# Kernel optimization log

Hardware: AMD Instinct MI355X
Metric: run time of the kernel (lower is better)

The kernel has to match this reference:

```python
import jax, jax.numpy as jnp
import numpy as np


def setup_inputs() -> dict:
    key = jax.random.key(0)
    k1, k2, k3 = jax.random.split(key, 3)
    B, D, H, W, K = 16, 512, 60, 60, 32
    std = 1.0 / np.sqrt(K * D)
    X = jax.random.normal(k1, (B, D, H, W), dtype=jnp.float32)
    codewords = jax.random.uniform(k2, (K, D), dtype=jnp.float32, minval=-std, maxval=std)
    # scale is drawn uniform(-1, 0) in the torch module (shake in train mode)
    scale = -jax.random.uniform(k3, (K,), dtype=jnp.float32)
    return {"X": X, "codewords": codewords, "scale": scale}


def reference(X, codewords, scale):
    # X: (B, D, H, W) -> flatten spatial to (B, N, D)
    B, D = X.shape[0], X.shape[1]
    Xf = X.reshape(B, D, -1).transpose(0, 2, 1)          # (B, N, D)
    # scaledL2: SL[b,n,k] = scale[k] * ||X[b,n] - C[k]||^2, expanded via GEMM
    # to avoid the (B, N, K, D) residual tensor.
    x2 = jnp.sum(Xf * Xf, axis=-1)                       # (B, N)
    c2 = jnp.sum(codewords * codewords, axis=-1)         # (K,)
    xc = jnp.einsum('bnd,kd->bnk', Xf, codewords)        # (B, N, K)
    sl = scale * (x2[..., None] - 2.0 * xc + c2)         # (B, N, K)
    A = jax.nn.softmax(sl, axis=2)                       # (B, N, K)
    # aggregate: E[b,k,d] = sum_n A[b,n,k] * (X[b,n,d] - C[k,d])
    E = jnp.einsum('bnk,bnd->bkd', A, Xf) - jnp.sum(A, axis=1)[..., None] * codewords
    return E                                             # (B, K, D)
```

## Files before the change

### kernel.cpp

```cpp
#include <hip/hip_runtime.h>
#include <hip/hip_bf16.h>

constexpr int BB = 16;
constexpr int DD = 512;
constexpr int NN = 3600;
constexpr int KK = 32;
constexpr int SB = 29;
constexpr int WIN = 128;

typedef __attribute__((ext_vector_type(8))) short short8;
typedef __attribute__((ext_vector_type(4))) float f32x4;

__device__ inline unsigned bf16pack(float a, float b) {
    unsigned ia = __float_as_uint(a), ib = __float_as_uint(b);
    ia = (ia + 0x7fffu + ((ia >> 16) & 1u)) >> 16;
    ib = (ib + 0x7fffu + ((ib >> 16) & 1u)) & 0xffff0000u;
    return ia | ib;
}

__global__ __launch_bounds__(256) void k0_prep(const float* __restrict__ Cw,
                                               const float* __restrict__ scale,
                                               ushort* __restrict__ Cbf,
                                               float* __restrict__ sc2) {
    __shared__ float buf[8][32];
    const int t = threadIdx.x;
    const int k = t & 31;
    const int h = t >> 5;
    const float4* row = reinterpret_cast<const float4*>(Cw + k * DD + h * 64);
    uint2* crow = reinterpret_cast<uint2*>(Cbf + k * DD + h * 64);
    float s = 0.f;
#pragma unroll
    for (int j = 0; j < 16; ++j) {
        float4 v = row[j];
        crow[j] = make_uint2(bf16pack(v.x, v.y), bf16pack(v.z, v.w));
        s += v.x * v.x + v.y * v.y + v.z * v.z + v.w * v.w;
    }
    buf[h][k] = s;
    __syncthreads();
    if (t < 32) {
        float tot = 0.f;
#pragma unroll
        for (int j = 0; j < 8; ++j) tot += buf[j][t];
        sc2[t] = scale[t] * tot;
    }
}

__global__ __launch_bounds__(512) void kf_fused(const float* __restrict__ X,
                                                const ushort* __restrict__ Cbf,
                                                const float* __restrict__ scale,
                                                const float* __restrict__ sc2,
                                                float* __restrict__ Ep,
                                                float* __restrict__ asum_part) {
    __shared__ ushort tile[DD * WIN];
    __shared__ ushort As2[KK * WIN];
    __shared__ float x2part[16][WIN];
    __shared__ float x2s[WIN];
    __shared__ float asw[8][KK];

    const int t = threadIdx.x;
    const int w = t >> 6;
    const int l = t & 63;
    const int q = l >> 4;
    const int r = l & 15;
    const int b = blockIdx.x / SB;
    const int sb = blockIdx.x % SB;
    const int n0 = sb * WIN;

    const int ng = t & 31;
    const int dgs = t >> 5;
    int nst = n0 + ng * 4;
    if (nst > NN - 4) nst = NN - 4;
    const float* xsrc = X + (size_t)b * DD * NN + nst;

    const ushort* cb0 = Cbf + r * DD + q * 8;
    const ushort* cb1 = cb0 + 16 * DD;
    const int nloc = w * 16 + r;

    float x2loc[4] = {0.f, 0.f, 0.f, 0.f};
    f32x4 a0 = {0.f, 0.f, 0.f, 0.f};
    f32x4 a1 = {0.f, 0.f, 0.f, 0.f};

    float4 cur[4];
#pragma unroll
    for (int i = 0; i < 4; ++i)
        cur[i] = *reinterpret_cast<const float4*>(xsrc + (size_t)(dgs * 4 + i) * NN);

#pragma unroll
    for (int j = 0; j < 8; ++j) {
        float4 nxt[4];
        if (j < 7) {
#pragma unroll
            for (int i = 0; i < 4; ++i)
                nxt[i] = *reinterpret_cast<const float4*>(
                    xsrc + (size_t)((j + 1) * 64 + dgs * 4 + i) * NN);
        }
#pragma unroll
        for (int i = 0; i < 4; ++i) {
            const float4 v = cur[i];
            x2loc[0] = fmaf(v.x, v.x, x2loc[0]);
            x2loc[1] = fmaf(v.y, v.y, x2loc[1]);
            x2loc[2] = fmaf(v.z, v.z, x2loc[2]);
            x2loc[3] = fmaf(v.w, v.w, x2loc[3]);
            const int d = j * 64 + dgs * 4 + i;
            *reinterpret_cast<uint2*>(&tile[d * 128 + ((ng * 4) ^ ((d & 7) << 3))]) =
                make_uint2(bf16pack(v.x, v.y), bf16pack(v.z, v.w));
        }
        __syncthreads();
#pragma unroll
        for (int u = 0; u < 2; ++u) {
            const int s = 2 * j + u;
            union { short8 s8; ushort us[8]; } af;
#pragma unroll
            for (int jj = 0; jj < 8; ++jj) {
                const int d = s * 32 + q * 8 + jj;
                af.us[jj] = tile[d * 128 + (nloc ^ (jj << 3))];
            }
            const short8 c0 = *reinterpret_cast<const short8*>(cb0 + s * 32);
            const short8 c1 = *reinterpret_cast<const short8*>(cb1 + s * 32);
            a0 = __builtin_amdgcn_mfma_f32_16x16x32_bf16(af.s8, c0, a0, 0, 0, 0);
            a1 = __builtin_amdgcn_mfma_f32_16x16x32_bf16(af.s8, c1, a1, 0, 0, 0);
        }
        if (j < 7) {
#pragma unroll
            for (int i = 0; i < 4; ++i) cur[i] = nxt[i];
        }
    }

    *reinterpret_cast<f32x4*>(&x2part[dgs][ng * 4]) =
        (f32x4){x2loc[0], x2loc[1], x2loc[2], x2loc[3]};
    __syncthreads();
    if (t < WIN) {
        float s = 0.f;
#pragma unroll
        for (int dg = 0; dg < 16; ++dg) s += x2part[dg][t];
        x2s[t] = s;
    }
    __syncthreads();

    const float sk0 = scale[r], sk1 = scale[r + 16];
    const float sq0 = sc2[r],  sq1 = sc2[r + 16];
    float e0v[4], e1v[4];
    float as0 = 0.f, as1 = 0.f;
#pragma unroll
    for (int i = 0; i < 4; ++i) {
        const float x2v = x2s[w * 16 + 4 * q + i];
        float sl0 = fmaf(sk0, x2v, sq0) - 2.f * sk0 * a0[i];
        float sl1 = fmaf(sk1, x2v, sq1) - 2.f * sk1 * a1[i];
        float m = fmaxf(sl0, sl1);
        m = fmaxf(m, __shfl_xor(m, 1));
        m = fmaxf(m, __shfl_xor(m, 2));
        m = fmaxf(m, __shfl_xor(m, 4));
        m = fmaxf(m, __shfl_xor(m, 8));
        float e0 = __expf(sl0 - m), e1 = __expf(sl1 - m);
        float ssum = e0 + e1;
        ssum += __shfl_xor(ssum, 1);
        ssum += __shfl_xor(ssum, 2);
        ssum += __shfl_xor(ssum, 4);
        ssum += __shfl_xor(ssum, 8);
        const float inv = 1.f / ssum;
        e0 *= inv; e1 *= inv;
        if (n0 + w * 16 + 4 * q + i >= NN) { e0 = 0.f; e1 = 0.f; }
        e0v[i] = e0; e1v[i] = e1;
        as0 += e0; as1 += e1;
    }
    *reinterpret_cast<uint2*>(&As2[r * 128 + ((w * 16 + 4 * q) ^ ((r & 7) << 3))]) =
        make_uint2(bf16pack(e0v[0], e0v[1]), bf16pack(e0v[2], e0v[3]));
    *reinterpret_cast<uint2*>(&As2[(r + 16) * 128 + ((w * 16 + 4 * q) ^ ((r & 7) << 3))]) =
        make_uint2(bf16pack(e1v[0], e1v[1]), bf16pack(e1v[2], e1v[3]));

    as0 += __shfl_xor(as0, 16); as0 += __shfl_xor(as0, 32);
    as1 += __shfl_xor(as1, 16); as1 += __shfl_xor(as1, 32);
    if (l < 16) { asw[w][r] = as0; asw[w][r + 16] = as1; }
    __syncthreads();
    if (t < KK) {
        float s = 0.f;
#pragma unroll
        for (int jw = 0; jw < 8; ++jw) s += asw[jw][t];
        asum_part[((size_t)b * SB + sb) * KK + t] = s;
    }

    short8 bfr0[4], bfr1[4];
#pragma unroll
    for (int step = 0; step < 4; ++step) {
        bfr0[step] = *reinterpret_cast<const short8*>(
            &As2[r * 128 + ((step * 32 + q * 8) ^ ((r & 7) << 3))]);
        bfr1[step] = *reinterpret_cast<const short8*>(
            &As2[(r + 16) * 128 + ((step * 32 + q * 8) ^ ((r & 7) << 3))]);
    }

    f32x4 acc[4][2];
#pragma unroll
    for (int df = 0; df < 4; ++df) {
        acc[df][0] = (f32x4){0.f, 0.f, 0.f, 0.f};
        acc[df][1] = (f32x4){0.f, 0.f, 0.f, 0.f};
    }

#pragma unroll
    for (int df = 0; df < 4; ++df) {
        const int d = w * 64 + df * 16 + r;
#pragma unroll
        for (int step = 0; step < 4; ++step) {
            const short8 xa = *reinterpret_cast<const short8*>(
                &tile[d * 128 + ((step * 32 + q * 8) ^ ((r & 7) << 3))]);
            acc[df][0] = __builtin_amdgcn_mfma_f32_16x16x32_bf16(
                xa, bfr0[step], acc[df][0], 0, 0, 0);
            acc[df][1] = __builtin_amdgcn_mfma_f32_16x16x32_bf16(
                xa, bfr1[step], acc[df][1], 0, 0, 0);
        }
    }

    float* ep = Ep + (size_t)(b * SB + sb) * KK * DD;
#pragma unroll
    for (int df = 0; df < 4; ++df) {
#pragma unroll
        for (int kf = 0; kf < 2; ++kf) {
            const int k = kf * 16 + r;
            const int d = w * 64 + df * 16 + q * 4;
            *reinterpret_cast<f32x4*>(ep + (size_t)k * DD + d) = acc[df][kf];
        }
    }
}

__global__ __launch_bounds__(256) void k3_final(const float* __restrict__ Ep,
                                                const float* __restrict__ asum_part,
                                                const float* __restrict__ Cw,
                                                float* __restrict__ E) {
    const int t = threadIdx.x;
    const int b = blockIdx.x >> 5, k = blockIdx.x & 31;

    float asum = 0.f;
#pragma unroll
    for (int sb = 0; sb < SB; ++sb)
        asum += asum_part[((size_t)b * SB + sb) * KK + k];

#pragma unroll
    for (int h = 0; h < 2; ++h) {
        const int d = t + h * 256;
        float s2 = 0.f;
#pragma unroll 4
        for (int sb = 0; sb < SB; ++sb)
            s2 += Ep[(((size_t)b * SB + sb) * KK + k) * DD + d];
        E[((size_t)b * KK + k) * DD + d] = s2 - asum * Cw[k * DD + d];
    }
}

extern "C" void kernel_launch(void* const* d_in, const int* in_sizes, int n_in,
                              void* d_out, int out_size, void* d_ws, size_t ws_size,
                              hipStream_t stream) {
    const float* X     = (const float*)d_in[0];
    const float* Cw    = (const float*)d_in[1];
    const float* scale = (const float*)d_in[2];
    float* E = (float*)d_out;

    float* ws = (float*)d_ws;
    float* Ep = ws;
    float* asum_part = Ep + (size_t)BB * SB * KK * DD;
    float* sc2 = asum_part + (size_t)BB * SB * KK;
    ushort* Cbf = (ushort*)(sc2 + KK);

    k0_prep<<<dim3(1), dim3(256), 0, stream>>>(Cw, scale, Cbf, sc2);
    kf_fused<<<dim3(BB * SB), dim3(512), 0, stream>>>(X, Cbf, scale, sc2, Ep, asum_part);
    k3_final<<<dim3(BB * KK), dim3(256), 0, stream>>>(Ep, asum_part, Cw, E);
}
```

Measured before the change: 59.51 us.

## Halve block size and LDS tile, process each 128-point window in two passes

The fused kernel now runs 256 threads per block. Each block handles its 128 spatial positions as two 64-wide passes, keeping the aggregation accumulators in registers across both passes. The LDS tile shrinks from 128 KB to about 68 KB, with padded strides (68/72) replacing the XOR swizzle. The intent is to fit more blocks per CU and raise occupancy. In exchange each wave holds twice the accumulators, so register pressure rises, and each pass adds barriers with less latency hiding per block.

```diff
diff --git a/kernel.cpp b/kernel.cpp
--- a/kernel.cpp
+++ b/kernel.cpp
@@ -6,7 +6,10 @@
 constexpr int NN = 3600;
 constexpr int KK = 32;
 constexpr int SB = 29;
-constexpr int WIN = 128;
+constexpr int WIN = 64;
+constexpr int PASSES = 2;
+constexpr int TS = 68;
+constexpr int AS = 72;
 
 typedef __attribute__((ext_vector_type(8))) short short8;
 typedef __attribute__((ext_vector_type(4))) float f32x4;
@@ -45,177 +48,178 @@
     }
 }
 
-__global__ __launch_bounds__(512) void kf_fused(const float* __restrict__ X,
+__global__ __launch_bounds__(256) void kf_fused(const float* __restrict__ X,
                                                 const ushort* __restrict__ Cbf,
                                                 const float* __restrict__ scale,
                                                 const float* __restrict__ sc2,
                                                 float* __restrict__ Ep,
                                                 float* __restrict__ asum_part) {
-    __shared__ ushort tile[DD * WIN];
-    __shared__ ushort As2[KK * WIN];
+    __shared__ ushort tile[DD * TS];
+    __shared__ ushort As2[KK * AS];
     __shared__ float x2part[16][WIN];
     __shared__ float x2s[WIN];
-    __shared__ float asw[8][KK];
+    __shared__ float asw[4][KK];
 
     const int t = threadIdx.x;
     const int w = t >> 6;
     const int l = t & 63;
     const int q = l >> 4;
     const int r = l & 15;
+    const int ng = t & 15;
+    const int dd = t >> 4;
     const int b = blockIdx.x / SB;
     const int sb = blockIdx.x % SB;
-    const int n0 = sb * WIN;
-
-    const int ng = t & 31;
-    const int dgs = t >> 5;
-    int nst = n0 + ng * 4;
-    if (nst > NN - 4) nst = NN - 4;
-    const float* xsrc = X + (size_t)b * DD * NN + nst;
-
+    const float* Xb = X + (size_t)b * DD * NN;
     const ushort* cb0 = Cbf + r * DD + q * 8;
     const ushort* cb1 = cb0 + 16 * DD;
-    const int nloc = w * 16 + r;
-
-    float x2loc[4] = {0.f, 0.f, 0.f, 0.f};
-    f32x4 a0 = {0.f, 0.f, 0.f, 0.f};
-    f32x4 a1 = {0.f, 0.f, 0.f, 0.f};
-
-    float4 cur[4];
-#pragma unroll
-    for (int i = 0; i < 4; ++i)
-        cur[i] = *reinterpret_cast<const float4*>(xsrc + (size_t)(dgs * 4 + i) * NN);
-
-#pragma unroll
-    for (int j = 0; j < 8; ++j) {
-        float4 nxt[4];
-        if (j < 7) {
-#pragma unroll
-            for (int i = 0; i < 4; ++i)
-                nxt[i] = *reinterpret_cast<const float4*>(
-                    xsrc + (size_t)((j + 1) * 64 + dgs * 4 + i) * NN);
-        }
-#pragma unroll
-        for (int i = 0; i < 4; ++i) {
-            const float4 v = cur[i];
-            x2loc[0] = fmaf(v.x, v.x, x2loc[0]);
-            x2loc[1] = fmaf(v.y, v.y, x2loc[1]);
-            x2loc[2] = fmaf(v.z, v.z, x2loc[2]);
-            x2loc[3] = fmaf(v.w, v.w, x2loc[3]);
-            const int d = j * 64 + dgs * 4 + i;
-            *reinterpret_cast<uint2*>(&tile[d * 128 + ((ng * 4) ^ ((d & 7) << 3))]) =
-                make_uint2(bf16pack(v.x, v.y), bf16pack(v.z, v.w));
-        }
-        __syncthreads();
-#pragma unroll
-        for (int u = 0; u < 2; ++u) {
-            const int s = 2 * j + u;
-            union { short8 s8; ushort us[8]; } af;
-#pragma unroll
-            for (int jj = 0; jj < 8; ++jj) {
-                const int d = s * 32 + q * 8 + jj;
-                af.us[jj] = tile[d * 128 + (nloc ^ (jj << 3))];
-            }
-            const short8 c0 = *reinterpret_cast<const short8*>(cb0 + s * 32);
-            const short8 c1 = *reinterpret_cast<const short8*>(cb1 + s * 32);
-            a0 = __builtin_amdgcn_mfma_f32_16x16x32_bf16(af.s8, c0, a0, 0, 0, 0);
-            a1 = __builtin_amdgcn_mfma_f32_16x16x32_bf16(af.s8, c1, a1, 0, 0, 0);
-        }
-        if (j < 7) {
-#pragma unroll
-            for (int i = 0; i < 4; ++i) cur[i] = nxt[i];
-        }
-    }
-
-    *reinterpret_cast<f32x4*>(&x2part[dgs][ng * 4]) =
-        (f32x4){x2loc[0], x2loc[1], x2loc[2], x2loc[3]};
-    __syncthreads();
-    if (t < WIN) {
-        float s = 0.f;
-#pragma unroll
-        for (int dg = 0; dg < 16; ++dg) s += x2part[dg][t];
-        x2s[t] = s;
-    }
-    __syncthreads();
-
     const float sk0 = scale[r], sk1 = scale[r + 16];
     const float sq0 = sc2[r],  sq1 = sc2[r + 16];
-    float e0v[4], e1v[4];
-    float as0 = 0.f, as1 = 0.f;
-#pragma unroll
-    for (int i = 0; i < 4; ++i) {
-        const float x2v = x2s[w * 16 + 4 * q + i];
-        float sl0 = fmaf(sk0, x2v, sq0) - 2.f * sk0 * a0[i];
-        float sl1 = fmaf(sk1, x2v, sq1) - 2.f * sk1 * a1[i];
-        float m = fmaxf(sl0, sl1);
-        m = fmaxf(m, __shfl_xor(m, 1));
-        m = fmaxf(m, __shfl_xor(m, 2));
-        m = fmaxf(m, __shfl_xor(m, 4));
-        m = fmaxf(m, __shfl_xor(m, 8));
-        float e0 = __expf(sl0 - m), e1 = __expf(sl1 - m);
-        float ssum = e0 + e1;
-        ssum += __shfl_xor(ssum, 1);
-        ssum += __shfl_xor(ssum, 2);
-        ssum += __shfl_xor(ssum, 4);
-        ssum += __shfl_xor(ssum, 8);
-        const float inv = 1.f / ssum;
-        e0 *= inv; e1 *= inv;
-        if (n0 + w * 16 + 4 * q + i >= NN) { e0 = 0.f; e1 = 0.f; }
-        e0v[i] = e0; e1v[i] = e1;
-        as0 += e0; as1 += e1;
-    }
-    *reinterpret_cast<uint2*>(&As2[r * 128 + ((w * 16 + 4 * q) ^ ((r & 7) << 3))]) =
-        make_uint2(bf16pack(e0v[0], e0v[1]), bf16pack(e0v[2], e0v[3]));
-    *reinterpret_cast<uint2*>(&As2[(r + 16) * 128 + ((w * 16 + 4 * q) ^ ((r & 7) << 3))]) =
-        make_uint2(bf16pack(e1v[0], e1v[1]), bf16pack(e1v[2], e1v[3]));
-
-    as0 += __shfl_xor(as0, 16); as0 += __shfl_xor(as0, 32);
-    as1 += __shfl_xor(as1, 16); as1 += __shfl_xor(as1, 32);
-    if (l < 16) { asw[w][r] = as0; asw[w][r + 16] = as1; }
+
+    f32x4 acc[8][2];
+#pragma unroll
+    for (int df = 0; df < 8; ++df) {
+        acc[df][0] = (f32x4){0.f, 0.f, 0.f, 0.f};
+        acc[df][1] = (f32x4){0.f, 0.f, 0.f, 0.f};
+    }
+    float as0t = 0.f, as1t = 0.f;
+
+    for (int p = 0; p < PASSES; ++p) {
+        const int n0p = sb * 128 + p * WIN;
+        int nst = n0p + ng * 4;
+        if (nst > NN - 4) nst = NN - 4;
+        const float* xsrc = Xb + nst;
+
+        f32x4 a0 = {0.f, 0.f, 0.f, 0.f};
+        f32x4 a1 = {0.f, 0.f, 0.f, 0.f};
+        float x2loc[4] = {0.f, 0.f, 0.f, 0.f};
+
+        float4 cur[4];
+#pragma unroll
+        for (int i = 0; i < 4; ++i)
+            cur[i] = *reinterpret_cast<const float4*>(xsrc + (size_t)(dd * 4 + i) * NN);
+
+        for (int c = 0; c < 8; ++c) {
+            float4 nxt[4];
+            if (c < 7) {
+#pragma unroll
+                for (int i = 0; i < 4; ++i)
+                    nxt[i] = *reinterpret_cast<const float4*>(
+                        xsrc + (size_t)((c + 1) * 64 + dd * 4 + i) * NN);
+            }
+#pragma unroll
+            for (int i = 0; i < 4; ++i) {
+                const float4 v = cur[i];
+                x2loc[0] = fmaf(v.x, v.x, x2loc[0]);
+                x2loc[1] = fmaf(v.y, v.y, x2loc[1]);
+                x2loc[2] = fmaf(v.z, v.z, x2loc[2]);
+                x2loc[3] = fmaf(v.w, v.w, x2loc[3]);
+                const int d = c * 64 + dd * 4 + i;
+                *reinterpret_cast<uint2*>(&tile[d * TS + ng * 4]) =
+                    make_uint2(bf16pack(v.x, v.y), bf16pack(v.z, v.w));
+            }
+            __syncthreads();
+#pragma unroll
+            for (int u = 0; u < 2; ++u) {
+                const int s = 2 * c + u;
+                union { short8 s8; ushort us[8]; } af;
+#pragma unroll
+                for (int jj = 0; jj < 8; ++jj)
+                    af.us[jj] = tile[(s * 32 + q * 8 + jj) * TS + w * 16 + r];
+                const short8 c0 = *reinterpret_cast<const short8*>(cb0 + s * 32);
+                const short8 c1 = *reinterpret_cast<const short8*>(cb1 + s * 32);
+                a0 = __builtin_amdgcn_mfma_f32_16x16x32_bf16(af.s8, c0, a0, 0, 0, 0);
+                a1 = __builtin_amdgcn_mfma_f32_16x16x32_bf16(af.s8, c1, a1, 0, 0, 0);
+            }
+            if (c < 7) {
+#pragma unroll
+                for (int i = 0; i < 4; ++i) cur[i] = nxt[i];
+            }
+        }
+
+        *reinterpret_cast<f32x4*>(&x2part[dd][ng * 4]) =
+            (f32x4){x2loc[0], x2loc[1], x2loc[2], x2loc[3]};
+        __syncthreads();
+        if (t < WIN) {
+            float s = 0.f;
+#pragma unroll
+            for (int dg = 0; dg < 16; ++dg) s += x2part[dg][t];
+            x2s[t] = s;
+        }
+        __syncthreads();
+
+        float e0v[4], e1v[4];
+#pragma unroll
+        for (int i = 0; i < 4; ++i) {
+            const float x2v = x2s[w * 16 + 4 * q + i];
+            float sl0 = fmaf(sk0, x2v, sq0) - 2.f * sk0 * a0[i];
+            float sl1 = fmaf(sk1, x2v, sq1) - 2.f * sk1 * a1[i];
+            float m = fmaxf(sl0, sl1);
+            m = fmaxf(m, __shfl_xor(m, 1));
+            m = fmaxf(m, __shfl_xor(m, 2));
+            m = fmaxf(m, __shfl_xor(m, 4));
+            m = fmaxf(m, __shfl_xor(m, 8));
+            float e0 = __expf(sl0 - m), e1 = __expf(sl1 - m);
+            float ssum = e0 + e1;
+            ssum += __shfl_xor(ssum, 1);
+            ssum += __shfl_xor(ssum, 2);
+            ssum += __shfl_xor(ssum, 4);
+            ssum += __shfl_xor(ssum, 8);
+            const float inv = 1.f / ssum;
+            e0 *= inv; e1 *= inv;
+            if (n0p + w * 16 + 4 * q + i >= NN) { e0 = 0.f; e1 = 0.f; }
+            e0v[i] = e0; e1v[i] = e1;
+            as0t += e0; as1t += e1;
+        }
+        *reinterpret_cast<uint2*>(&As2[r * AS + w * 16 + 4 * q]) =
+            make_uint2(bf16pack(e0v[0], e0v[1]), bf16pack(e0v[2], e0v[3]));
+        *reinterpret_cast<uint2*>(&As2[(r + 16) * AS + w * 16 + 4 * q]) =
+            make_uint2(bf16pack(e1v[0], e1v[1]), bf16pack(e1v[2], e1v[3]));
+        __syncthreads();
+
+        short8 bfr0[2], bfr1[2];
+#pragma unroll
+        for (int step = 0; step < 2; ++step) {
+            bfr0[step] = *reinterpret_cast<const short8*>(
+                &As2[r * AS + step * 32 + q * 8]);
+            bfr1[step] = *reinterpret_cast<const short8*>(
+                &As2[(r + 16) * AS + step * 32 + q * 8]);
+        }
+#pragma unroll
+        for (int df = 0; df < 8; ++df) {
+            const int d = w * 128 + df * 16 + r;
+#pragma unroll
+            for (int step = 0; step < 2; ++step) {
+                union { short8 s8; uint2 u2[2]; } xa;
+                const ushort* tp = &tile[d * TS + step * 32 + q * 8];
+                xa.u2[0] = *reinterpret_cast<const uint2*>(tp);
+                xa.u2[1] = *reinterpret_cast<const uint2*>(tp + 4);
+                acc[df][0] = __builtin_amdgcn_mfma_f32_16x16x32_bf16(
+                    xa.s8, bfr0[step], acc[df][0], 0, 0, 0);
+                acc[df][1] = __builtin_amdgcn_mfma_f32_16x16x32_bf16(
+                    xa.s8, bfr1[step], acc[df][1], 0, 0, 0);
+            }
+        }
+        __syncthreads();
+    }
+
+    as0t += __shfl_xor(as0t, 16); as0t += __shfl_xor(as0t, 32);
+    as1t += __shfl_xor(as1t, 16); as1t += __shfl_xor(as1t, 32);
+    if (l < 16) { asw[w][r] = as0t; asw[w][r + 16] = as1t; }
     __syncthreads();
     if (t < KK) {
         float s = 0.f;
 #pragma unroll
-        for (int jw = 0; jw < 8; ++jw) s += asw[jw][t];
+        for (int jw = 0; jw < 4; ++jw) s += asw[jw][t];
         asum_part[((size_t)b * SB + sb) * KK + t] = s;
     }
 
-    short8 bfr0[4], bfr1[4];
-#pragma unroll
-    for (int step = 0; step < 4; ++step) {
-        bfr0[step] = *reinterpret_cast<const short8*>(
-            &As2[r * 128 + ((step * 32 + q * 8) ^ ((r & 7) << 3))]);
-        bfr1[step] = *reinterpret_cast<const short8*>(
-            &As2[(r + 16) * 128 + ((step * 32 + q * 8) ^ ((r & 7) << 3))]);
-    }
-
-    f32x4 acc[4][2];
-#pragma unroll
-    for (int df = 0; df < 4; ++df) {
-        acc[df][0] = (f32x4){0.f, 0.f, 0.f, 0.f};
-        acc[df][1] = (f32x4){0.f, 0.f, 0.f, 0.f};
-    }
-
-#pragma unroll
-    for (int df = 0; df < 4; ++df) {
-        const int d = w * 64 + df * 16 + r;
-#pragma unroll
-        for (int step = 0; step < 4; ++step) {
-            const short8 xa = *reinterpret_cast<const short8*>(
-                &tile[d * 128 + ((step * 32 + q * 8) ^ ((r & 7) << 3))]);
-            acc[df][0] = __builtin_amdgcn_mfma_f32_16x16x32_bf16(
-                xa, bfr0[step], acc[df][0], 0, 0, 0);
-            acc[df][1] = __builtin_amdgcn_mfma_f32_16x16x32_bf16(
-                xa, bfr1[step], acc[df][1], 0, 0, 0);
-        }
-    }
-
     float* ep = Ep + (size_t)(b * SB + sb) * KK * DD;
 #pragma unroll
-    for (int df = 0; df < 4; ++df) {
+    for (int df = 0; df < 8; ++df) {
 #pragma unroll
         for (int kf = 0; kf < 2; ++kf) {
             const int k = kf * 16 + r;
-            const int d = w * 64 + df * 16 + q * 4;
+            const int d = w * 128 + df * 16 + q * 4;
             *reinterpret_cast<f32x4*>(ep + (size_t)k * DD + d) = acc[df][kf];
         }
     }
@@ -259,6 +263,6 @@
     ushort* Cbf = (ushort*)(sc2 + KK);
 
     k0_prep<<<dim3(1), dim3(256), 0, stream>>>(Cw, scale, Cbf, sc2);
-    kf_fused<<<dim3(BB * SB), dim3(512), 0, stream>>>(X, Cbf, scale, sc2, Ep, asum_part);
+    kf_fused<<<dim3(BB * SB), dim3(256), 0, stream>>>(X, Cbf, scale, sc2, Ep, asum_part);
     k3_final<<<dim3(BB * KK), dim3(256), 0, stream>>>(Ep, asum_part, Cw, E);
 }
```

After: 66.76 us. 12.2% more time.

## Load X in four 128-row chunks with double-buffered prefetch and fewer barriers

Applied to the files above, without the earlier changes.

The first phase now loads X in four chunks of 128 D-rows, each thread holding 8 float4 loads in a ping-pong register buffer, instead of eight chunks of 64 rows. This halves the number of block barriers and puts more global loads in flight per chunk. Codeword fragments are loaded at the top of each chunk, and a raw s_barrier plus sched_barrier replace __syncthreads. Launch bounds now ask for 2 blocks per CU, which raises register pressure from the larger buffers. The swizzle index in the second GEMM changes from (r&7) to (d&7), which is equivalent because d ≡ r mod 8.

```diff
diff --git a/kernel.cpp b/kernel.cpp
--- a/kernel.cpp
+++ b/kernel.cpp
@@ -45,12 +45,12 @@
     }
 }
 
-__global__ __launch_bounds__(512) void kf_fused(const float* __restrict__ X,
-                                                const ushort* __restrict__ Cbf,
-                                                const float* __restrict__ scale,
-                                                const float* __restrict__ sc2,
-                                                float* __restrict__ Ep,
-                                                float* __restrict__ asum_part) {
+__global__ __launch_bounds__(512, 2) void kf_fused(const float* __restrict__ X,
+                                                   const ushort* __restrict__ Cbf,
+                                                   const float* __restrict__ scale,
+                                                   const float* __restrict__ sc2,
+                                                   float* __restrict__ Ep,
+                                                   float* __restrict__ asum_part) {
     __shared__ ushort tile[DD * WIN];
     __shared__ ushort As2[KK * WIN];
     __shared__ float x2part[16][WIN];
@@ -62,69 +62,75 @@
     const int l = t & 63;
     const int q = l >> 4;
     const int r = l & 15;
+    const int ng = t & 31;
+    const int dgs = t >> 5;
     const int b = blockIdx.x / SB;
     const int sb = blockIdx.x % SB;
     const int n0 = sb * WIN;
-
-    const int ng = t & 31;
-    const int dgs = t >> 5;
+    const float* Xb = X + (size_t)b * DD * NN;
+    const ushort* cb0 = Cbf + r * DD + q * 8;
+    const ushort* cb1 = cb0 + 16 * DD;
+
     int nst = n0 + ng * 4;
     if (nst > NN - 4) nst = NN - 4;
-    const float* xsrc = X + (size_t)b * DD * NN + nst;
-
-    const ushort* cb0 = Cbf + r * DD + q * 8;
-    const ushort* cb1 = cb0 + 16 * DD;
+    const float* xsrc = Xb + nst;
+
     const int nloc = w * 16 + r;
-
-    float x2loc[4] = {0.f, 0.f, 0.f, 0.f};
     f32x4 a0 = {0.f, 0.f, 0.f, 0.f};
     f32x4 a1 = {0.f, 0.f, 0.f, 0.f};
-
-    float4 cur[4];
-#pragma unroll
-    for (int i = 0; i < 4; ++i)
-        cur[i] = *reinterpret_cast<const float4*>(xsrc + (size_t)(dgs * 4 + i) * NN);
-
-#pragma unroll
-    for (int j = 0; j < 8; ++j) {
-        float4 nxt[4];
-        if (j < 7) {
-#pragma unroll
-            for (int i = 0; i < 4; ++i)
-                nxt[i] = *reinterpret_cast<const float4*>(
-                    xsrc + (size_t)((j + 1) * 64 + dgs * 4 + i) * NN);
-        }
-#pragma unroll
-        for (int i = 0; i < 4; ++i) {
-            const float4 v = cur[i];
-            x2loc[0] = fmaf(v.x, v.x, x2loc[0]);
-            x2loc[1] = fmaf(v.y, v.y, x2loc[1]);
-            x2loc[2] = fmaf(v.z, v.z, x2loc[2]);
-            x2loc[3] = fmaf(v.w, v.w, x2loc[3]);
-            const int d = j * 64 + dgs * 4 + i;
-            *reinterpret_cast<uint2*>(&tile[d * 128 + ((ng * 4) ^ ((d & 7) << 3))]) =
-                make_uint2(bf16pack(v.x, v.y), bf16pack(v.z, v.w));
-        }
-        __syncthreads();
-#pragma unroll
-        for (int u = 0; u < 2; ++u) {
-            const int s = 2 * j + u;
-            union { short8 s8; ushort us[8]; } af;
-#pragma unroll
-            for (int jj = 0; jj < 8; ++jj) {
-                const int d = s * 32 + q * 8 + jj;
-                af.us[jj] = tile[d * 128 + (nloc ^ (jj << 3))];
-            }
-            const short8 c0 = *reinterpret_cast<const short8*>(cb0 + s * 32);
-            const short8 c1 = *reinterpret_cast<const short8*>(cb1 + s * 32);
-            a0 = __builtin_amdgcn_mfma_f32_16x16x32_bf16(af.s8, c0, a0, 0, 0, 0);
-            a1 = __builtin_amdgcn_mfma_f32_16x16x32_bf16(af.s8, c1, a1, 0, 0, 0);
-        }
-        if (j < 7) {
-#pragma unroll
-            for (int i = 0; i < 4; ++i) cur[i] = nxt[i];
-        }
-    }
+    float x2loc[4] = {0.f, 0.f, 0.f, 0.f};
+
+    float4 bufA[8], bufB[8];
+#pragma unroll
+    for (int i = 0; i < 8; ++i)
+        bufA[i] = *reinterpret_cast<const float4*>(xsrc + (size_t)(dgs * 8 + i) * NN);
+
+#define CHUNK_BODY(CURB, NXTB, C)                                              \
+    {                                                                          \
+        short8 cf0[4], cf1[4];                                                 \
+        _Pragma("unroll")                                                      \
+        for (int u = 0; u < 4; ++u) {                                          \
+            cf0[u] = *reinterpret_cast<const short8*>(cb0 + ((C)*4 + u) * 32); \
+            cf1[u] = *reinterpret_cast<const short8*>(cb1 + ((C)*4 + u) * 32); \
+        }                                                                      \
+        if ((C) < 3) {                                                         \
+            _Pragma("unroll")                                                  \
+            for (int i = 0; i < 8; ++i)                                        \
+                NXTB[i] = *reinterpret_cast<const float4*>(                    \
+                    xsrc + (size_t)(((C) + 1) * 128 + dgs * 8 + i) * NN);      \
+        }                                                                      \
+        _Pragma("unroll")                                                      \
+        for (int i = 0; i < 8; ++i) {                                          \
+            const float4 v = CURB[i];                                          \
+            x2loc[0] = fmaf(v.x, v.x, x2loc[0]);                               \
+            x2loc[1] = fmaf(v.y, v.y, x2loc[1]);                               \
+            x2loc[2] = fmaf(v.z, v.z, x2loc[2]);                               \
+            x2loc[3] = fmaf(v.w, v.w, x2loc[3]);                               \
+            const int d = (C) * 128 + dgs * 8 + i;                             \
+            *reinterpret_cast<uint2*>(                                         \
+                &tile[d * WIN + ((ng * 4) ^ ((d & 7) << 3))]) =                \
+                make_uint2(bf16pack(v.x, v.y), bf16pack(v.z, v.w));            \
+        }                                                                      \
+        asm volatile("s_waitcnt lgkmcnt(0)" ::: "memory");                     \
+        __builtin_amdgcn_s_barrier();                                          \
+        __builtin_amdgcn_sched_barrier(0);                                     \
+        _Pragma("unroll")                                                      \
+        for (int u = 0; u < 4; ++u) {                                          \
+            const int s = (C) * 4 + u;                                         \
+            union { short8 s8; ushort us[8]; } af;                             \
+            _Pragma("unroll")                                                  \
+            for (int jj = 0; jj < 8; ++jj)                                     \
+                af.us[jj] = tile[(s * 32 + q * 8 + jj) * WIN + (nloc ^ (jj << 3))]; \
+            a0 = __builtin_amdgcn_mfma_f32_16x16x32_bf16(af.s8, cf0[u], a0, 0, 0, 0); \
+            a1 = __builtin_amdgcn_mfma_f32_16x16x32_bf16(af.s8, cf1[u], a1, 0, 0, 0); \
+        }                                                                      \
+    }
+
+    CHUNK_BODY(bufA, bufB, 0)
+    CHUNK_BODY(bufB, bufA, 1)
+    CHUNK_BODY(bufA, bufB, 2)
+    CHUNK_BODY(bufB, bufA, 3)
+#undef CHUNK_BODY
 
     *reinterpret_cast<f32x4*>(&x2part[dgs][ng * 4]) =
         (f32x4){x2loc[0], x2loc[1], x2loc[2], x2loc[3]};
@@ -163,9 +169,9 @@
         e0v[i] = e0; e1v[i] = e1;
         as0 += e0; as1 += e1;
     }
-    *reinterpret_cast<uint2*>(&As2[r * 128 + ((w * 16 + 4 * q) ^ ((r & 7) << 3))]) =
+    *reinterpret_cast<uint2*>(&As2[r * WIN + ((w * 16 + 4 * q) ^ ((r & 7) << 3))]) =
         make_uint2(bf16pack(e0v[0], e0v[1]), bf16pack(e0v[2], e0v[3]));
-    *reinterpret_cast<uint2*>(&As2[(r + 16) * 128 + ((w * 16 + 4 * q) ^ ((r & 7) << 3))]) =
+    *reinterpret_cast<uint2*>(&As2[(r + 16) * WIN + ((w * 16 + 4 * q) ^ ((r & 7) << 3))]) =
         make_uint2(bf16pack(e1v[0], e1v[1]), bf16pack(e1v[2], e1v[3]));
 
     as0 += __shfl_xor(as0, 16); as0 += __shfl_xor(as0, 32);
@@ -183,9 +189,9 @@
 #pragma unroll
     for (int step = 0; step < 4; ++step) {
         bfr0[step] = *reinterpret_cast<const short8*>(
-            &As2[r * 128 + ((step * 32 + q * 8) ^ ((r & 7) << 3))]);
+            &As2[r * WIN + ((step * 32 + q * 8) ^ ((r & 7) << 3))]);
         bfr1[step] = *reinterpret_cast<const short8*>(
-            &As2[(r + 16) * 128 + ((step * 32 + q * 8) ^ ((r & 7) << 3))]);
+            &As2[(r + 16) * WIN + ((step * 32 + q * 8) ^ ((r & 7) << 3))]);
     }
 
     f32x4 acc[4][2];
@@ -201,7 +207,7 @@
 #pragma unroll
         for (int step = 0; step < 4; ++step) {
             const short8 xa = *reinterpret_cast<const short8*>(
-                &tile[d * 128 + ((step * 32 + q * 8) ^ ((r & 7) << 3))]);
+                &tile[d * WIN + ((step * 32 + q * 8) ^ ((d & 7) << 3))]);
             acc[df][0] = __builtin_amdgcn_mfma_f32_16x16x32_bf16(
                 xa, bfr0[step], acc[df][0], 0, 0, 0);
             acc[df][1] = __builtin_amdgcn_mfma_f32_16x16x32_bf16(
```

Measured after the change: 57.95 us. -2.6%, faster.

## Warp-specialize fused kernel into producer and MFMA consumer waves with LDS flags

Applied to the files above, without the earlier changes.

Splits the 8 waves into 4 producer waves that load X, compute x2 and write the bf16 tile, and 4 consumer waves that spin on per-chunk LDS flags and run the distance MFMAs and softmax. This replaces the per-chunk block-wide __syncthreads with fine-grained flag signalling, so global loads can overlap with matrix work. It also changes the LDS swizzle key to mix higher row bits, aiming to cut bank conflicts. The cost is that only half the waves do each phase, and correctness now depends on spin-wait flags and on lgkmcnt ordering.

```diff
diff --git a/kernel.cpp b/kernel.cpp
--- a/kernel.cpp
+++ b/kernel.cpp
@@ -16,6 +16,10 @@
     ia = (ia + 0x7fffu + ((ia >> 16) & 1u)) >> 16;
     ib = (ib + 0x7fffu + ((ib >> 16) & 1u)) & 0xffff0000u;
     return ia | ib;
+}
+
+__device__ inline int swzkey(int row) {
+    return ((row ^ (row >> 3)) & 7) << 3;
 }
 
 __global__ __launch_bounds__(256) void k0_prep(const float* __restrict__ Cw,
@@ -53,9 +57,10 @@
                                                 float* __restrict__ asum_part) {
     __shared__ ushort tile[DD * WIN];
     __shared__ ushort As2[KK * WIN];
-    __shared__ float x2part[16][WIN];
+    __shared__ float x2part[8][WIN];
     __shared__ float x2s[WIN];
-    __shared__ float asw[8][KK];
+    __shared__ float asw[4][KK];
+    __shared__ int flags[8][4];
 
     const int t = threadIdx.x;
     const int w = t >> 6;
@@ -65,117 +70,156 @@
     const int b = blockIdx.x / SB;
     const int sb = blockIdx.x % SB;
     const int n0 = sb * WIN;
-
-    const int ng = t & 31;
-    const int dgs = t >> 5;
-    int nst = n0 + ng * 4;
-    if (nst > NN - 4) nst = NN - 4;
-    const float* xsrc = X + (size_t)b * DD * NN + nst;
-
-    const ushort* cb0 = Cbf + r * DD + q * 8;
-    const ushort* cb1 = cb0 + 16 * DD;
-    const int nloc = w * 16 + r;
-
-    float x2loc[4] = {0.f, 0.f, 0.f, 0.f};
-    f32x4 a0 = {0.f, 0.f, 0.f, 0.f};
-    f32x4 a1 = {0.f, 0.f, 0.f, 0.f};
-
-    float4 cur[4];
-#pragma unroll
-    for (int i = 0; i < 4; ++i)
-        cur[i] = *reinterpret_cast<const float4*>(xsrc + (size_t)(dgs * 4 + i) * NN);
-
-#pragma unroll
-    for (int j = 0; j < 8; ++j) {
-        float4 nxt[4];
-        if (j < 7) {
-#pragma unroll
-            for (int i = 0; i < 4; ++i)
-                nxt[i] = *reinterpret_cast<const float4*>(
-                    xsrc + (size_t)((j + 1) * 64 + dgs * 4 + i) * NN);
-        }
-#pragma unroll
-        for (int i = 0; i < 4; ++i) {
-            const float4 v = cur[i];
-            x2loc[0] = fmaf(v.x, v.x, x2loc[0]);
-            x2loc[1] = fmaf(v.y, v.y, x2loc[1]);
-            x2loc[2] = fmaf(v.z, v.z, x2loc[2]);
-            x2loc[3] = fmaf(v.w, v.w, x2loc[3]);
-            const int d = j * 64 + dgs * 4 + i;
-            *reinterpret_cast<uint2*>(&tile[d * 128 + ((ng * 4) ^ ((d & 7) << 3))]) =
-                make_uint2(bf16pack(v.x, v.y), bf16pack(v.z, v.w));
-        }
-        __syncthreads();
-#pragma unroll
-        for (int u = 0; u < 2; ++u) {
-            const int s = 2 * j + u;
-            union { short8 s8; ushort us[8]; } af;
-#pragma unroll
-            for (int jj = 0; jj < 8; ++jj) {
-                const int d = s * 32 + q * 8 + jj;
-                af.us[jj] = tile[d * 128 + (nloc ^ (jj << 3))];
+    const float* Xb = X + (size_t)b * DD * NN;
+
+    if (t < 32) flags[t >> 2][t & 3] = 0;
+    __syncthreads();
+
+    if (w < 4) {
+        const int p = w;
+        const int ng = l & 31;
+        const int dr = l >> 5;
+        const int rbase = p * 16 + dr * 8;
+        int nst = n0 + ng * 4;
+        if (nst > NN - 4) nst = NN - 4;
+        const float* xsrc = Xb + nst;
+        float x2loc[4] = {0.f, 0.f, 0.f, 0.f};
+
+        float4 bufA[8], bufB[8];
+#pragma unroll
+        for (int i = 0; i < 8; ++i)
+            bufA[i] = *reinterpret_cast<const float4*>(xsrc + (size_t)(rbase + i) * NN);
+
+#define PROD_CHUNK(CURB, NXTB, C)                                              \
+        {                                                                      \
+            if ((C) < 7) {                                                     \
+                _Pragma("unroll")                                              \
+                for (int i = 0; i < 8; ++i)                                    \
+                    NXTB[i] = *reinterpret_cast<const float4*>(                \
+                        xsrc + (size_t)(((C) + 1) * 64 + rbase + i) * NN);     \
+            }                                                                  \
+            _Pragma("unroll")                                                  \
+            for (int i = 0; i < 8; ++i) {                                      \
+                const float4 v = CURB[i];                                      \
+                x2loc[0] = fmaf(v.x, v.x, x2loc[0]);                           \
+                x2loc[1] = fmaf(v.y, v.y, x2loc[1]);                           \
+                x2loc[2] = fmaf(v.z, v.z, x2loc[2]);                           \
+                x2loc[3] = fmaf(v.w, v.w, x2loc[3]);                           \
+                const int d = (C) * 64 + rbase + i;                            \
+                *reinterpret_cast<uint2*>(                                     \
+                    &tile[d * WIN + ((ng * 4) ^ swzkey(d))]) =                 \
+                    make_uint2(bf16pack(v.x, v.y), bf16pack(v.z, v.w));        \
+            }                                                                  \
+            if ((C) == 7)                                                      \
+                *reinterpret_cast<f32x4*>(&x2part[p * 2 + dr][ng * 4]) =       \
+                    (f32x4){x2loc[0], x2loc[1], x2loc[2], x2loc[3]};           \
+            asm volatile("s_waitcnt lgkmcnt(0)" ::: "memory");                 \
+            if (l == 0) *(volatile int*)&flags[(C)][p] = 1;                    \
+        }
+        PROD_CHUNK(bufA, bufB, 0)
+        PROD_CHUNK(bufB, bufA, 1)
+        PROD_CHUNK(bufA, bufB, 2)
+        PROD_CHUNK(bufB, bufA, 3)
+        PROD_CHUNK(bufA, bufB, 4)
+        PROD_CHUNK(bufB, bufA, 5)
+        PROD_CHUNK(bufA, bufB, 6)
+        PROD_CHUNK(bufB, bufA, 7)
+#undef PROD_CHUNK
+    } else {
+        const int cw = w - 4;
+        const int nbase = cw * 32;
+        const ushort* cb0 = Cbf + r * DD + q * 8;
+        const ushort* cb1 = cb0 + 16 * DD;
+
+        f32x4 aA0 = {0.f,0.f,0.f,0.f}, aA1 = {0.f,0.f,0.f,0.f};
+        f32x4 aB0 = {0.f,0.f,0.f,0.f}, aB1 = {0.f,0.f,0.f,0.f};
+
+        for (int c = 0; c < 8; ++c) {
+            short8 cf0[2], cf1[2];
+#pragma unroll
+            for (int u = 0; u < 2; ++u) {
+                cf0[u] = *reinterpret_cast<const short8*>(cb0 + (c * 2 + u) * 32);
+                cf1[u] = *reinterpret_cast<const short8*>(cb1 + (c * 2 + u) * 32);
             }
-            const short8 c0 = *reinterpret_cast<const short8*>(cb0 + s * 32);
-            const short8 c1 = *reinterpret_cast<const short8*>(cb1 + s * 32);
-            a0 = __builtin_amdgcn_mfma_f32_16x16x32_bf16(af.s8, c0, a0, 0, 0, 0);
-            a1 = __builtin_amdgcn_mfma_f32_16x16x32_bf16(af.s8, c1, a1, 0, 0, 0);
-        }
-        if (j < 7) {
-#pragma unroll
-            for (int i = 0; i < 4; ++i) cur[i] = nxt[i];
-        }
-    }
-
-    *reinterpret_cast<f32x4*>(&x2part[dgs][ng * 4]) =
-        (f32x4){x2loc[0], x2loc[1], x2loc[2], x2loc[3]};
+            volatile int* vf = &flags[c][0];
+            while (!(vf[0] & vf[1] & vf[2] & vf[3]))
+                __builtin_amdgcn_s_sleep(1);
+            asm volatile("" ::: "memory");
+            __builtin_amdgcn_sched_barrier(0);
+#pragma unroll
+            for (int u = 0; u < 2; ++u) {
+                const int s = c * 2 + u;
+                union { short8 s8; ushort us[8]; } af0, af1;
+#pragma unroll
+                for (int jj = 0; jj < 8; ++jj) {
+                    const int dA = s * 32 + q * 8 + jj;
+                    const int key = swzkey(dA);
+                    af0.us[jj] = tile[dA * WIN + ((nbase + r) ^ key)];
+                    af1.us[jj] = tile[dA * WIN + ((nbase + 16 + r) ^ key)];
+                }
+                aA0 = __builtin_amdgcn_mfma_f32_16x16x32_bf16(af0.s8, cf0[u], aA0, 0, 0, 0);
+                aA1 = __builtin_amdgcn_mfma_f32_16x16x32_bf16(af0.s8, cf1[u], aA1, 0, 0, 0);
+                aB0 = __builtin_amdgcn_mfma_f32_16x16x32_bf16(af1.s8, cf0[u], aB0, 0, 0, 0);
+                aB1 = __builtin_amdgcn_mfma_f32_16x16x32_bf16(af1.s8, cf1[u], aB1, 0, 0, 0);
+            }
+        }
+
+        if (l < 32) {
+            float s = 0.f;
+#pragma unroll
+            for (int j = 0; j < 8; ++j) s += x2part[j][nbase + l];
+            x2s[nbase + l] = s;
+        }
+
+        const float sk0 = scale[r], sk1 = scale[r + 16];
+        const float sq0 = sc2[r],  sq1 = sc2[r + 16];
+        float as0 = 0.f, as1 = 0.f;
+#define SOFTMAX_FRAG(A0, A1, F)                                                \
+        {                                                                      \
+            float e0v[4], e1v[4];                                              \
+            _Pragma("unroll")                                                  \
+            for (int i = 0; i < 4; ++i) {                                      \
+                const float x2v = x2s[nbase + (F) * 16 + 4 * q + i];           \
+                float sl0 = fmaf(sk0, x2v, sq0) - 2.f * sk0 * A0[i];           \
+                float sl1 = fmaf(sk1, x2v, sq1) - 2.f * sk1 * A1[i];           \
+                float m = fmaxf(sl0, sl1);                                     \
+                m = fmaxf(m, __shfl_xor(m, 1));                                \
+                m = fmaxf(m, __shfl_xor(m, 2));                                \
+                m = fmaxf(m, __shfl_xor(m, 4));                                \
+                m = fmaxf(m, __shfl_xor(m, 8));                                \
+                float e0 = __expf(sl0 - m), e1 = __expf(sl1 - m);              \
+                float ssum = e0 + e1;                                          \
+                ssum += __shfl_xor(ssum, 1);                                   \
+                ssum += __shfl_xor(ssum, 2);                                   \
+                ssum += __shfl_xor(ssum, 4);                                   \
+                ssum += __shfl_xor(ssum, 8);                                   \
+                const float inv = 1.f / ssum;                                  \
+                e0 *= inv; e1 *= inv;                                          \
+                if (n0 + nbase + (F) * 16 + 4 * q + i >= NN) { e0 = 0.f; e1 = 0.f; } \
+                e0v[i] = e0; e1v[i] = e1;                                      \
+                as0 += e0; as1 += e1;                                          \
+            }                                                                  \
+            const int ncol = nbase + (F) * 16 + 4 * q;                         \
+            *reinterpret_cast<uint2*>(&As2[r * WIN + (ncol ^ swzkey(r))]) =    \
+                make_uint2(bf16pack(e0v[0], e0v[1]), bf16pack(e0v[2], e0v[3]));\
+            *reinterpret_cast<uint2*>(&As2[(r + 16) * WIN + (ncol ^ swzkey(r + 16))]) = \
+                make_uint2(bf16pack(e1v[0], e1v[1]), bf16pack(e1v[2], e1v[3]));\
+        }
+        SOFTMAX_FRAG(aA0, aA1, 0)
+        SOFTMAX_FRAG(aB0, aB1, 1)
+#undef SOFTMAX_FRAG
+
+        as0 += __shfl_xor(as0, 16); as0 += __shfl_xor(as0, 32);
+        as1 += __shfl_xor(as1, 16); as1 += __shfl_xor(as1, 32);
+        if (l < 16) { asw[cw][r] = as0; asw[cw][r + 16] = as1; }
+    }
+
     __syncthreads();
-    if (t < WIN) {
-        float s = 0.f;
-#pragma unroll
-        for (int dg = 0; dg < 16; ++dg) s += x2part[dg][t];
-        x2s[t] = s;
-    }
-    __syncthreads();
-
-    const float sk0 = scale[r], sk1 = scale[r + 16];
-    const float sq0 = sc2[r],  sq1 = sc2[r + 16];
-    float e0v[4], e1v[4];
-    float as0 = 0.f, as1 = 0.f;
-#pragma unroll
-    for (int i = 0; i < 4; ++i) {
-        const float x2v = x2s[w * 16 + 4 * q + i];
-        float sl0 = fmaf(sk0, x2v, sq0) - 2.f * sk0 * a0[i];
-        float sl1 = fmaf(sk1, x2v, sq1) - 2.f * sk1 * a1[i];
-        float m = fmaxf(sl0, sl1);
-        m = fmaxf(m, __shfl_xor(m, 1));
-        m = fmaxf(m, __shfl_xor(m, 2));
-        m = fmaxf(m, __shfl_xor(m, 4));
-        m = fmaxf(m, __shfl_xor(m, 8));
-        float e0 = __expf(sl0 - m), e1 = __expf(sl1 - m);
-        float ssum = e0 + e1;
-        ssum += __shfl_xor(ssum, 1);
-        ssum += __shfl_xor(ssum, 2);
-        ssum += __shfl_xor(ssum, 4);
-        ssum += __shfl_xor(ssum, 8);
-        const float inv = 1.f / ssum;
-        e0 *= inv; e1 *= inv;
-        if (n0 + w * 16 + 4 * q + i >= NN) { e0 = 0.f; e1 = 0.f; }
-        e0v[i] = e0; e1v[i] = e1;
-        as0 += e0; as1 += e1;
-    }
-    *reinterpret_cast<uint2*>(&As2[r * 128 + ((w * 16 + 4 * q) ^ ((r & 7) << 3))]) =
-        make_uint2(bf16pack(e0v[0], e0v[1]), bf16pack(e0v[2], e0v[3]));
-    *reinterpret_cast<uint2*>(&As2[(r + 16) * 128 + ((w * 16 + 4 * q) ^ ((r & 7) << 3))]) =
-        make_uint2(bf16pack(e1v[0], e1v[1]), bf16pack(e1v[2], e1v[3]));
-
-    as0 += __shfl_xor(as0, 16); as0 += __shfl_xor(as0, 32);
-    as1 += __shfl_xor(as1, 16); as1 += __shfl_xor(as1, 32);
-    if (l < 16) { asw[w][r] = as0; asw[w][r + 16] = as1; }
-    __syncthreads();
+
     if (t < KK) {
         float s = 0.f;
 #pragma unroll
-        for (int jw = 0; jw < 8; ++jw) s += asw[jw][t];
+        for (int j = 0; j < 4; ++j) s += asw[j][t];
         asum_part[((size_t)b * SB + sb) * KK + t] = s;
     }
 
@@ -183,9 +227,9 @@
 #pragma unroll
     for (int step = 0; step < 4; ++step) {
         bfr0[step] = *reinterpret_cast<const short8*>(
-            &As2[r * 128 + ((step * 32 + q * 8) ^ ((r & 7) << 3))]);
+            &As2[r * WIN + ((step * 32 + q * 8) ^ swzkey(r))]);
         bfr1[step] = *reinterpret_cast<const short8*>(
-            &As2[(r + 16) * 128 + ((step * 32 + q * 8) ^ ((r & 7) << 3))]);
+            &As2[(r + 16) * WIN + ((step * 32 + q * 8) ^ swzkey(r + 16))]);
     }
 
     f32x4 acc[4][2];
@@ -198,10 +242,11 @@
 #pragma unroll
     for (int df = 0; df < 4; ++df) {
         const int d = w * 64 + df * 16 + r;
+        const int kd = swzkey(d);
 #pragma unroll
         for (int step = 0; step < 4; ++step) {
             const short8 xa = *reinterpret_cast<const short8*>(
-                &tile[d * 128 + ((step * 32 + q * 8) ^ ((r & 7) << 3))]);
+                &tile[d * WIN + ((step * 32 + q * 8) ^ kd)]);
             acc[df][0] = __builtin_amdgcn_mfma_f32_16x16x32_bf16(
                 xa, bfr0[step], acc[df][0], 0, 0, 0);
             acc[df][1] = __builtin_amdgcn_mfma_f32_16x16x32_bf16(
```

After: 66.50 us. +11.7%, slower.
